# Kernel optimization log

Hardware: AMD Instinct MI355X
Metric: run time of the kernel (lower is better)

The kernel has to match this reference:

```python
import math
import jax, jax.numpy as jnp
import numpy as np

# ---- matryoshka config (matches init_kwargs) ----
NUM_HEADS = 16
KV_GROUPS = 4
KV_REPEATS = NUM_HEADS // KV_GROUPS
QK_SIZES = [32, 64, 128]      # output_sizes // num_heads
HEAD_SIZES = [32, 64, 128]
D_MODEL = 2048
NEG_INF = -1e9


def _heads_reorder_indices(num_heads, sizes, reverse=False):
    parts = [[] for _ in range(num_heads)]
    offset, prev = 0, 0
    for size in sizes:
        seg = size - prev
        for h in range(num_heads):
            parts[h].append(np.arange(offset, offset + seg))
            offset += seg
        prev = size
    reorder = np.concatenate([a for head in parts for a in head])
    if reverse:
        rev = np.empty_like(reorder)
        rev[reorder] = np.arange(len(reorder))
        reorder = rev
    return jnp.asarray(reorder, dtype=jnp.int32)

Q_REORDER = _heads_reorder_indices(NUM_HEADS, QK_SIZES)
K_REORDER = _heads_reorder_indices(KV_GROUPS, QK_SIZES)
V_REORDER = _heads_reorder_indices(KV_GROUPS, HEAD_SIZES)
O_REORDER = _heads_reorder_indices(NUM_HEADS, HEAD_SIZES, reverse=True)


def setup_inputs() -> dict:
    key = jax.random.key(0)
    ks = jax.random.split(key, 9)
    B, S = 2, 1024
    dq = NUM_HEADS * QK_SIZES[-1]      # 2048
    dkv_q = KV_GROUPS * QK_SIZES[-1]   # 512
    dkv_v = KV_GROUPS * HEAD_SIZES[-1] # 512
    dout = NUM_HEADS * HEAD_SIZES[-1]  # 2048
    s = 0.02
    return {
        "x": jax.random.normal(ks[0], (B, S, D_MODEL), jnp.float32),
        "mask": jnp.tril(jnp.ones((S, S), jnp.bool_)),
        "Wq": jax.random.normal(ks[1], (D_MODEL, dq), jnp.float32) * s,
        "bq": jnp.zeros((dq,), jnp.float32),
        "Wk": jax.random.normal(ks[2], (D_MODEL, dkv_q), jnp.float32) * s,
        "bk": jnp.zeros((dkv_q,), jnp.float32),
        "Wv": jax.random.normal(ks[3], (D_MODEL, dkv_v), jnp.float32) * s,
        "bv": jnp.zeros((dkv_v,), jnp.float32),
        "Wo": jax.random.normal(ks[4], (dout, D_MODEL), jnp.float32) * s,
        "bo": jnp.zeros((D_MODEL,), jnp.float32),
    }


def reference(x, mask, Wq, bq, Wk, bk, Wv, bv, Wo, bo):
    B, S, _ = x.shape
    H, G, R = NUM_HEADS, KV_GROUPS, KV_REPEATS
    Dq, Dh = QK_SIZES[-1], HEAD_SIZES[-1]

    # matryoshka projections (full-size forward) + buffer-indexed reorder
    q = (x @ Wq + bq)[..., Q_REORDER]
    k = (x @ Wk + bk)[..., K_REORDER]
    v = (x @ Wv + bv)[..., V_REORDER]

    q = q.reshape(B, S, H, Dq).transpose(0, 2, 1, 3)   # [B,H,S,Dq]
    k = k.reshape(B, S, G, Dq).transpose(0, 2, 1, 3)   # [B,G,S,Dq]
    v = v.reshape(B, S, G, Dh).transpose(0, 2, 1, 3)   # [B,G,S,Dh]

    # GQA expansion: each group repeated kv_repeats times consecutively
    k = jnp.repeat(k, R, axis=1)  # [B,H,S,Dq]
    v = jnp.repeat(v, R, axis=1)  # [B,H,S,Dh]

    add_mask = jnp.where(mask, 0.0, NEG_INF).astype(x.dtype)  # [S,S]

    xs = []
    dp_cum = 0.0
    prev_qk, prev_hd = 0, 0
    for qk, hd in zip(QK_SIZES, HEAD_SIZES):
        # dot product over the NEW qk segment, accumulated over prefixes
        dp = jnp.einsum('bhqd,bhkd->bhqk', q[..., prev_qk:qk], k[..., prev_qk:qk])
        dp_cum = dp_cum + dp
        logits = dp_cum * (1.0 / math.sqrt(qk)) + add_mask
        attn = jax.nn.softmax(logits, axis=-1)
        # output only the NEW value segment for this nesting level
        xs.append(jnp.einsum('bhqk,bhkd->bhqd', attn, v[..., prev_hd:hd]))
        prev_qk, prev_hd = qk, hd

    out = jnp.concatenate(xs, axis=-1)                 # [B,H,S,Dh]
    out = out.transpose(0, 2, 1, 3).reshape(B, S, H * Dh)
    out = out[..., O_REORDER]
    return out @ Wo + bo
```

## Files before the change

### kernel.cpp

```cpp
#include <hip/hip_runtime.h>

typedef __attribute__((ext_vector_type(8))) __bf16 bf16x8;
typedef __attribute__((ext_vector_type(8))) unsigned short u16x8;
typedef __attribute__((ext_vector_type(4))) float f32x4;

#define XBOFF 0
#define WQKVOFF (XBOFF + 2048 * 2048)
#define WOOFF   (WQKVOFF + 3072 * 2048)
#define QOFF    (WOOFF + 2048 * 2048)
#define KOFF    (QOFF + 2048 * 2048)
#define VTOFF   (KOFF + 2048 * 512)
#define AOFF    (VTOFF + 2048 * 512)
__device__ __align__(16) ushort g_scratch[AOFF + 2048 * 2048];

__device__ __forceinline__ int nest_map(int n, int H) {
    int h = n >> 7, j = n & 127;
    if (j < 32) return h * 32 + j;
    if (j < 64) return H * 32 + h * 32 + (j - 32);
    return H * 64 + h * 64 + (j - 64);
}

__device__ __forceinline__ ushort f2bf(float f) {
    unsigned u = __builtin_bit_cast(unsigned, f);
    u += 0x7fffu + ((u >> 16) & 1u);
    return (ushort)(u >> 16);
}
__device__ __forceinline__ bf16x8 ld_frag(const ushort* p) {
    return __builtin_bit_cast(bf16x8, *(const u16x8*)p);
}
__device__ __forceinline__ void glds16(const ushort* g, ushort* s) {
    __builtin_amdgcn_global_load_lds(
        (const __attribute__((address_space(1))) void*)g,
        (__attribute__((address_space(3))) void*)s, 16, 0, 0);
}

__global__ __launch_bounds__(256) void prep_kernel(
    const float* __restrict__ x,
    const float* __restrict__ Wq, const float* __restrict__ Wk,
    const float* __restrict__ Wv, const float* __restrict__ Wo)
{
    const int bx = blockIdx.x;
    const int tid = threadIdx.x;

    if (bx < 2048) {
        size_t i = ((size_t)bx * 256 + tid) * 8;
        float4 f0 = *(const float4*)&x[i];
        float4 f1 = *(const float4*)&x[i + 4];
        union { uint4 v; ushort u[8]; } a;
        a.u[0] = f2bf(f0.x); a.u[1] = f2bf(f0.y); a.u[2] = f2bf(f0.z); a.u[3] = f2bf(f0.w);
        a.u[4] = f2bf(f1.x); a.u[5] = f2bf(f1.y); a.u[6] = f2bf(f1.z); a.u[7] = f2bf(f1.w);
        *(uint4*)&g_scratch[XBOFF + i] = a.v;
        return;
    }

    const float* W; int rowlen, H, mode, dstoff, t;
    if (bx < 3072)      { W = Wq; rowlen = 2048; H = 16; mode = 0; dstoff = WQKVOFF;               t = bx - 2048; }
    else if (bx < 3328) { W = Wk; rowlen = 512;  H = 4;  mode = 0; dstoff = WQKVOFF + 2048 * 2048; t = bx - 3072; }
    else if (bx < 3584) { W = Wv; rowlen = 512;  H = 4;  mode = 0; dstoff = WQKVOFF + 2560 * 2048; t = bx - 3328; }
    else                { W = Wo; rowlen = 2048; H = 16; mode = 1; dstoff = WOOFF;                 t = bx - 3584; }
    const int k0 = (t & 31) * 64;
    const int n0 = (t >> 5) * 64;

    __shared__ ushort T[64][66];
    const int r = tid >> 3, oct = tid & 7;

    #pragma unroll
    for (int rep = 0; rep < 2; ++rep) {
        int rr = r + rep * 32;
        int wrow = mode ? nest_map(k0 + rr, 16) : (k0 + rr);
        int wcol = mode ? (n0 + oct * 8) : nest_map(n0 + oct * 8, H);
        float4 f0 = *(const float4*)&W[(size_t)wrow * rowlen + wcol];
        float4 f1 = *(const float4*)&W[(size_t)wrow * rowlen + wcol + 4];
        ushort* d = &T[rr][oct * 8];
        d[0] = f2bf(f0.x); d[1] = f2bf(f0.y); d[2] = f2bf(f0.z); d[3] = f2bf(f0.w);
        d[4] = f2bf(f1.x); d[5] = f2bf(f1.y); d[6] = f2bf(f1.z); d[7] = f2bf(f1.w);
    }
    __syncthreads();
    #pragma unroll
    for (int rep = 0; rep < 2; ++rep) {
        int rr = r + rep * 32;
        union { uint4 v; ushort u[8]; } cv;
        #pragma unroll
        for (int i = 0; i < 8; ++i) cv.u[i] = T[oct * 8 + i][rr];
        *(uint4*)&g_scratch[dstoff + (size_t)(n0 + rr) * 2048 + k0 + oct * 8] = cv.v;
    }
}

__global__ __launch_bounds__(256) void gemm128_kernel(
    const float* __restrict__ b0, const float* __restrict__ b1,
    const float* __restrict__ b2, float* __restrict__ oext, int mode)
{
    __shared__ __align__(16) ushort SH[2 * 12288];

    const int gx = gridDim.x;
    const int gy = gridDim.y;
    const int id = blockIdx.x + gx * blockIdx.y;
    const int xcd = id & 7, idl = id >> 3;
    const int CM = gy >> 1, CN = gx >> 2;
    const int m_idx = (xcd >> 2) * CM + (idl % CM);
    const int n_idx = (xcd & 3) * CN + (idl / CM);
    const int n0 = n_idx * 64;
    const int m0 = m_idx * 128;

    const int tid = threadIdx.x;
    const int lane = tid & 63, wid = tid >> 6;
    const int wm = wid & 1, wn = wid >> 1;
    const int quad = lane >> 4, l16 = lane & 15;

    const ushort* A  = g_scratch + (mode ? AOFF : XBOFF);
    const ushort* Bt = g_scratch + (mode ? WOOFF : WQKVOFF);

    const bool vpath = (mode == 0) && (n0 >= 2560);
    const float* bias; ushort* outS = nullptr; int c0, oldim, H;
    if (mode == 1)      { bias = b0; c0 = n0; oldim = 2048; H = 0; }
    else if (n0 < 2048) { bias = b0; outS = g_scratch + QOFF; c0 = n0;        oldim = 2048; H = 16; }
    else if (n0 < 2560) { bias = b1; outS = g_scratch + KOFF; c0 = n0 - 2048; oldim = 512;  H = 4; }
    else                { bias = b2; outS = nullptr;          c0 = n0 - 2560; oldim = 512;  H = 4; }

    const int lrow = lane >> 3;
    const int lchunk = (lane & 7) ^ (lrow & 7);

    f32x4 acc[4][2];
    #pragma unroll
    for (int a = 0; a < 4; ++a)
        #pragma unroll
        for (int c = 0; c < 2; ++c) acc[a][c] = f32x4{0.f, 0.f, 0.f, 0.f};

    auto STAGE = [&](int buf, int kt) {
        const int k0 = kt * 64;
        ushort* as_ = SH + buf * 12288;
        ushort* bs_ = as_ + 8192;
        #pragma unroll
        for (int it = 0; it < 4; ++it) {
            int rb = it * 32 + wid * 8;
            int r  = rb + lrow;
            glds16(&A[(size_t)(m0 + r) * 2048 + k0 + lchunk * 8], &as_[rb * 64]);
        }
        #pragma unroll
        for (int it = 0; it < 2; ++it) {
            int rb = it * 32 + wid * 8;
            int r  = rb + lrow;
            glds16(&Bt[(size_t)(n0 + r) * 2048 + k0 + lchunk * 8], &bs_[rb * 64]);
        }
    };

    STAGE(0, 0);
    STAGE(1, 1);

    for (int kt = 0; kt < 32; ++kt) {
        if (kt < 31) asm volatile("s_waitcnt vmcnt(6)" ::: "memory");
        else         asm volatile("s_waitcnt vmcnt(0)" ::: "memory");
        __builtin_amdgcn_s_barrier();

        const ushort* as_ = SH + (kt & 1) * 12288;
        const ushort* bs_ = as_ + 8192;
        #pragma unroll
        for (int kc = 0; kc < 2; ++kc) {
            bf16x8 af[4], bf[2];
            #pragma unroll
            for (int s = 0; s < 4; ++s) {
                int ra = wm * 64 + s * 16 + l16;
                int ch = kc * 4 + quad;
                af[s] = ld_frag(&as_[ra * 64 + ((ch ^ (ra & 7)) * 8)]);
            }
            #pragma unroll
            for (int s = 0; s < 2; ++s) {
                int rbv = wn * 32 + s * 16 + l16;
                int ch = kc * 4 + quad;
                bf[s] = ld_frag(&bs_[rbv * 64 + ((ch ^ (rbv & 7)) * 8)]);
            }
            #pragma unroll
            for (int sm = 0; sm < 4; ++sm)
                #pragma unroll
                for (int sn = 0; sn < 2; ++sn)
                    acc[sm][sn] = __builtin_amdgcn_mfma_f32_16x16x32_bf16(
                        af[sm], bf[sn], acc[sm][sn], 0, 0, 0);
        }
        __builtin_amdgcn_s_barrier();
        if (kt <= 29) STAGE(kt & 1, kt + 2);
    }
    __syncthreads();

    if (vpath) {
        #pragma unroll
        for (int sm = 0; sm < 4; ++sm)
        #pragma unroll
        for (int sn = 0; sn < 2; ++sn)
        #pragma unroll
        for (int i = 0; i < 4; ++i) {
            int r = wm * 64 + sm * 16 + quad * 4 + i;
            int loc = wn * 32 + sn * 16 + l16;
            float v = acc[sm][sn][i] + bias[nest_map(c0 + loc, 4)];
            SH[loc * 128 + (r ^ ((loc & 7) << 3))] = f2bf(v);
        }
        __syncthreads();
        const int dloc = tid >> 2;
        const int qcol = (tid & 3) * 32;
        const int gg = c0 >> 7, din = (c0 & 127);
        const int bb = m0 >> 10, sb = m0 & 1023;
        ushort* vt = g_scratch + VTOFF;
        #pragma unroll
        for (int j = 0; j < 4; ++j) {
            int r = qcol + j * 8;
            uint4 v = *(uint4*)&SH[dloc * 128 + (r ^ ((dloc & 7) << 3))];
            *(uint4*)&vt[((size_t)((bb * 4 + gg) * 128 + din + dloc)) * 1024 + sb + r] = v;
        }
    } else {
        #pragma unroll
        for (int sm = 0; sm < 4; ++sm)
        #pragma unroll
        for (int sn = 0; sn < 2; ++sn)
        #pragma unroll
        for (int i = 0; i < 4; ++i) {
            int row = m0 + wm * 64 + sm * 16 + quad * 4 + i;
            int loc = wn * 32 + sn * 16 + l16;
            float v = acc[sm][sn][i];
            if (mode == 1) {
                oext[(size_t)row * 2048 + c0 + loc] = v + bias[c0 + loc];
            } else {
                v += bias[nest_map(c0 + loc, H)];
                outS[(size_t)row * oldim + c0 + loc] = f2bf(v);
            }
        }
    }
}

__global__ __launch_bounds__(256) void attn_kernel()
{
    const ushort* qb = g_scratch + QOFF;
    const ushort* kb = g_scratch + KOFF;
    const ushort* vt = g_scratch + VTOFF;
    ushort* att = g_scratch + AOFF;

    __shared__ __align__(16) ushort Ks[64 * 128];
    __shared__ __align__(16) ushort Vt[128 * 64];
    __shared__ __align__(16) ushort Ps[64 * 64];

    const int x = blockIdx.x, h = blockIdx.y, b = blockIdx.z;
    const int ks_half = x >> 1;
    const int qt = ((x ^ b) & 1) ? ks_half : 15 - ks_half;
    const int g = h >> 2;
    const int q0 = qt * 64;
    const int tid = threadIdx.x;
    const int lane = tid & 63, w = tid >> 6;
    const int quad = lane >> 4, l16 = lane & 15;

    bf16x8 qa[4];
    {
        const ushort* qrow =
            qb + ((size_t)((b * 1024 + q0 + w * 16 + l16) * 16 + h)) * 128;
        #pragma unroll
        for (int kc = 0; kc < 4; ++kc)
            qa[kc] = ld_frag(qrow + kc * 32 + quad * 8);
    }

    float m_s[3][4], l_s[3][4];
    #pragma unroll
    for (int l = 0; l < 3; ++l)
        #pragma unroll
        for (int i = 0; i < 4; ++i) { m_s[l][i] = -1e9f; l_s[l][i] = 0.0f; }
    f32x4 oacc[8];
    #pragma unroll
    for (int t2 = 0; t2 < 8; ++t2) oacc[t2] = f32x4{0.f, 0.f, 0.f, 0.f};
    const f32x4 fz = {0.f, 0.f, 0.f, 0.f};
    const bf16x8 ones = __builtin_bit_cast(bf16x8, u16x8{
        0x3F80, 0x3F80, 0x3F80, 0x3F80, 0x3F80, 0x3F80, 0x3F80, 0x3F80});

    for (int kt = 0; kt <= qt; ++kt) {
        const int k0 = kt * 64;
        {
            int r16 = tid >> 4, oct16 = tid & 15;
            #pragma unroll
            for (int rep = 0; rep < 4; ++rep) {
                int row = r16 + rep * 16;
                *(uint4*)&Ks[row * 128 + ((oct16 ^ (row & 7)) * 8)] =
                    *(const uint4*)&kb[(size_t)((b * 1024 + k0 + row) * 4 + g) * 128 + oct16 * 8];
            }
            int oct = tid & 7, dr = tid >> 3;
            #pragma unroll
            for (int rep = 0; rep < 4; ++rep) {
                int d = dr + rep * 32;
                *(uint4*)&Vt[d * 64 + ((oct ^ (d & 7)) * 8)] =
                    *(const uint4*)&vt[((size_t)((b * 4 + g) * 128 + d)) * 1024 + k0 + oct * 8];
            }
        }
        __syncthreads();

        const bool diag = (kt == qt);

        f32x4 s0[4], s1[4], s2[4];
        __builtin_amdgcn_s_setprio(1);
        #pragma unroll
        for (int n = 0; n < 4; ++n) {
            int r = n * 16 + l16;
            s0[n] = __builtin_amdgcn_mfma_f32_16x16x32_bf16(
                qa[0], ld_frag(&Ks[r * 128 + (((0 + quad) ^ (r & 7)) * 8)]), fz, 0, 0, 0);
        }
        #pragma unroll
        for (int n = 0; n < 4; ++n) {
            int r = n * 16 + l16;
            s1[n] = __builtin_amdgcn_mfma_f32_16x16x32_bf16(
                qa[1], ld_frag(&Ks[r * 128 + (((4 + quad) ^ (r & 7)) * 8)]), s0[n], 0, 0, 0);
        }
        #pragma unroll
        for (int n = 0; n < 4; ++n) {
            int r = n * 16 + l16;
            s2[n] = __builtin_amdgcn_mfma_f32_16x16x32_bf16(
                qa[2], ld_frag(&Ks[r * 128 + (((8 + quad) ^ (r & 7)) * 8)]), s1[n], 0, 0, 0);
        }
        #pragma unroll
        for (int n = 0; n < 4; ++n) {
            int r = n * 16 + l16;
            s2[n] = __builtin_amdgcn_mfma_f32_16x16x32_bf16(
                qa[3], ld_frag(&Ks[r * 128 + (((12 + quad) ^ (r & 7)) * 8)]), s2[n], 0, 0, 0);
        }
        __builtin_amdgcn_s_setprio(0);

        float sv[3][4][4], mx[3][4];
        #pragma unroll
        for (int l = 0; l < 3; ++l)
            #pragma unroll
            for (int i = 0; i < 4; ++i) mx[l][i] = -1e9f;
        #pragma unroll
        for (int n = 0; n < 4; ++n)
            #pragma unroll
            for (int i = 0; i < 4; ++i) {
                bool msk = diag &&
                    (k0 + n * 16 + l16 > q0 + w * 16 + quad * 4 + i);
                float x0 = msk ? -1e9f : s0[n][i] * 0.1767766953f;
                float x1 = msk ? -1e9f : s1[n][i] * 0.125f;
                float x2 = msk ? -1e9f : s2[n][i] * 0.0883883476f;
                sv[0][n][i] = x0; mx[0][i] = fmaxf(mx[0][i], x0);
                sv[1][n][i] = x1; mx[1][i] = fmaxf(mx[1][i], x1);
                sv[2][n][i] = x2; mx[2][i] = fmaxf(mx[2][i], x2);
            }
        #pragma unroll
        for (int d = 1; d < 16; d <<= 1)
            #pragma unroll
            for (int l = 0; l < 3; ++l)
                #pragma unroll
                for (int i = 0; i < 4; ++i)
                    mx[l][i] = fmaxf(mx[l][i], __shfl_xor(mx[l][i], d, 64));
        float al[3][4];
        #pragma unroll
        for (int l = 0; l < 3; ++l)
            #pragma unroll
            for (int i = 0; i < 4; ++i) {
                float mn = fmaxf(m_s[l][i], mx[l][i]);
                al[l][i] = __expf(m_s[l][i] - mn);
                m_s[l][i] = mn;
            }
        #pragma unroll
        for (int n = 0; n < 4; ++n)
            #pragma unroll
            for (int l = 0; l < 3; ++l)
                #pragma unroll
                for (int i = 0; i < 4; ++i)
                    sv[l][n][i] = __expf(sv[l][n][i] - m_s[l][i]);
        #pragma unroll
        for (int t = 0; t < 8; ++t) {
            int lvl = (t < 2) ? 0 : (t < 4) ? 1 : 2;
            #pragma unroll
            for (int i = 0; i < 4; ++i) oacc[t][i] *= al[lvl][i];
        }

        f32x4 racc[3];
        const int obase[3] = {0, 2, 4}, onts[3] = {2, 2, 4}, voffs[3] = {0, 32, 64};
        #pragma unroll
        for (int l = 0; l < 3; ++l) {
            #pragma unroll
            for (int n = 0; n < 4; ++n)
                #pragma unroll
                for (int i = 0; i < 4; ++i) {
                    int prow = w * 16 + quad * 4 + i;
                    int col = n * 16 + l16;
                    Ps[prow * 64 + ((((col >> 3) ^ (prow & 7)) << 3) | (col & 7))] =
                        f2bf(sv[l][n][i]);
                }
            racc[l] = fz;
            __builtin_amdgcn_s_setprio(1);
            #pragma unroll
            for (int kc = 0; kc < 2; ++kc) {
                int prow = w * 16 + l16;
                bf16x8 pa = ld_frag(&Ps[prow * 64 + (((kc * 4 + quad) ^ (prow & 7)) * 8)]);
                racc[l] = __builtin_amdgcn_mfma_f32_16x16x32_bf16(
                    pa, ones, racc[l], 0, 0, 0);
                #pragma unroll
                for (int t = 0; t < 4; ++t) {
                    if (t < onts[l]) {
                        int vd = voffs[l] + t * 16 + l16;
                        bf16x8 vf = ld_frag(&Vt[vd * 64 + (((kc * 4 + quad) ^ (vd & 7)) * 8)]);
                        oacc[obase[l] + t] = __builtin_amdgcn_mfma_f32_16x16x32_bf16(
                            pa, vf, oacc[obase[l] + t], 0, 0, 0);
                    }
                }
            }
            __builtin_amdgcn_s_setprio(0);
        }
        #pragma unroll
        for (int l = 0; l < 3; ++l)
            #pragma unroll
            for (int i = 0; i < 4; ++i)
                l_s[l][i] = l_s[l][i] * al[l][i] + racc[l][i];
        __syncthreads();
    }

    float inv[3][4];
    #pragma unroll
    for (int l = 0; l < 3; ++l)
        #pragma unroll
        for (int i = 0; i < 4; ++i) {
            float L = l_s[l][i];
            inv[l][i] = (L > 0.f) ? (1.0f / L) : 0.f;
        }
    #pragma unroll
    for (int t = 0; t < 8; ++t) {
        int lvl = (t < 2) ? 0 : (t < 4) ? 1 : 2;
        #pragma unroll
        for (int i = 0; i < 4; ++i) {
            int srow = q0 + w * 16 + quad * 4 + i;
            att[(size_t)((b * 1024 + srow) * 16 + h) * 128 + t * 16 + l16] =
                f2bf(oacc[t][i] * inv[lvl][i]);
        }
    }
}

extern "C" void kernel_launch(void* const* d_in, const int* in_sizes, int n_in,
                              void* d_out, int out_size, void* d_ws, size_t ws_size,
                              hipStream_t stream)
{
    const float* x  = (const float*)d_in[0];
    const float* Wq = (const float*)d_in[2];
    const float* bq = (const float*)d_in[3];
    const float* Wk = (const float*)d_in[4];
    const float* bk = (const float*)d_in[5];
    const float* Wv = (const float*)d_in[6];
    const float* bv = (const float*)d_in[7];
    const float* Wo = (const float*)d_in[8];
    const float* bo = (const float*)d_in[9];
    float* out = (float*)d_out;
    (void)d_ws; (void)ws_size;

    dim3 blk(256, 1, 1);
    hipLaunchKernelGGL(prep_kernel, dim3(4608), blk, 0, stream, x, Wq, Wk, Wv, Wo);
    hipLaunchKernelGGL(gemm128_kernel, dim3(48, 16), blk, 0, stream,
                       bq, bk, bv, (float*)nullptr, 0);
    hipLaunchKernelGGL(attn_kernel, dim3(16, 16, 2), blk, 0, stream);
    hipLaunchKernelGGL(gemm128_kernel, dim3(32, 16), blk, 0, stream,
                       bo, nullptr, nullptr, out, 1);
}
```

Baseline: 261.3 us.

## Double-buffer K/V tiles in attention with async global-to-LDS loads

The attention kernel now keeps two LDS buffers each for K and V^T. The next key tile is prefetched with direct global-to-LDS loads (glds16) while the current tile is computed, and vmcnt waits plus raw s_barrier replace the register-staged copy and __syncthreads. The aim is to hide global load latency behind the MFMA work. In exchange LDS use roughly doubles, which may cut occupancy. The manual vmcnt counting is also fragile: if other outstanding loads change the count, the ordering can break.

```diff
diff --git a/kernel.cpp b/kernel.cpp
--- a/kernel.cpp
+++ b/kernel.cpp
@@ -232,8 +232,8 @@
     const ushort* vt = g_scratch + VTOFF;
     ushort* att = g_scratch + AOFF;
 
-    __shared__ __align__(16) ushort Ks[64 * 128];
-    __shared__ __align__(16) ushort Vt[128 * 64];
+    __shared__ __align__(16) ushort Ks[2][64 * 128];
+    __shared__ __align__(16) ushort Vt[2][128 * 64];
     __shared__ __align__(16) ushort Ps[64 * 64];
 
     const int x = blockIdx.x, h = blockIdx.y, b = blockIdx.z;
@@ -244,6 +244,27 @@
     const int tid = threadIdx.x;
     const int lane = tid & 63, w = tid >> 6;
     const int quad = lane >> 4, l16 = lane & 15;
+    const int w4 = w * 4, w8 = w * 8;
+
+    auto STAGE = [&](int bf, int kt) {
+        const int k0 = kt * 64;
+        #pragma unroll
+        for (int rep = 0; rep < 4; ++rep) {
+            int rowb = rep * 16 + w4;
+            int row  = rowb + (lane >> 4);
+            int c    = lane & 15;
+            glds16(&kb[(size_t)((b * 1024 + k0 + row) * 4 + g) * 128 + ((c ^ (row & 7)) * 8)],
+                   &Ks[bf][rowb * 128]);
+        }
+        #pragma unroll
+        for (int rep = 0; rep < 4; ++rep) {
+            int db = rep * 32 + w8;
+            int d  = db + (lane >> 3);
+            int c  = lane & 7;
+            glds16(&vt[((size_t)((b * 4 + g) * 128 + d)) * 1024 + k0 + ((c ^ (d & 7)) * 8)],
+                   &Vt[bf][db * 64]);
+        }
+    };
 
     bf16x8 qa[4];
     {
@@ -266,26 +287,20 @@
     const bf16x8 ones = __builtin_bit_cast(bf16x8, u16x8{
         0x3F80, 0x3F80, 0x3F80, 0x3F80, 0x3F80, 0x3F80, 0x3F80, 0x3F80});
 
+    STAGE(0, 0);
+
     for (int kt = 0; kt <= qt; ++kt) {
         const int k0 = kt * 64;
-        {
-            int r16 = tid >> 4, oct16 = tid & 15;
-            #pragma unroll
-            for (int rep = 0; rep < 4; ++rep) {
-                int row = r16 + rep * 16;
-                *(uint4*)&Ks[row * 128 + ((oct16 ^ (row & 7)) * 8)] =
-                    *(const uint4*)&kb[(size_t)((b * 1024 + k0 + row) * 4 + g) * 128 + oct16 * 8];
-            }
-            int oct = tid & 7, dr = tid >> 3;
-            #pragma unroll
-            for (int rep = 0; rep < 4; ++rep) {
-                int d = dr + rep * 32;
-                *(uint4*)&Vt[d * 64 + ((oct ^ (d & 7)) * 8)] =
-                    *(const uint4*)&vt[((size_t)((b * 4 + g) * 128 + d)) * 1024 + k0 + oct * 8];
-            }
-        }
-        __syncthreads();
-
+        if (kt < qt) {
+            STAGE((kt + 1) & 1, kt + 1);
+            asm volatile("s_waitcnt vmcnt(8)" ::: "memory");
+        } else {
+            asm volatile("s_waitcnt vmcnt(0)" ::: "memory");
+        }
+        __builtin_amdgcn_s_barrier();
+
+        const ushort* KsC = Ks[kt & 1];
+        const ushort* VtC = Vt[kt & 1];
         const bool diag = (kt == qt);
 
         f32x4 s0[4], s1[4], s2[4];
@@ -294,25 +309,25 @@
         for (int n = 0; n < 4; ++n) {
             int r = n * 16 + l16;
             s0[n] = __builtin_amdgcn_mfma_f32_16x16x32_bf16(
-                qa[0], ld_frag(&Ks[r * 128 + (((0 + quad) ^ (r & 7)) * 8)]), fz, 0, 0, 0);
+                qa[0], ld_frag(&KsC[r * 128 + (((0 + quad) ^ (r & 7)) * 8)]), fz, 0, 0, 0);
         }
         #pragma unroll
         for (int n = 0; n < 4; ++n) {
             int r = n * 16 + l16;
             s1[n] = __builtin_amdgcn_mfma_f32_16x16x32_bf16(
-                qa[1], ld_frag(&Ks[r * 128 + (((4 + quad) ^ (r & 7)) * 8)]), s0[n], 0, 0, 0);
+                qa[1], ld_frag(&KsC[r * 128 + (((4 + quad) ^ (r & 7)) * 8)]), s0[n], 0, 0, 0);
         }
         #pragma unroll
         for (int n = 0; n < 4; ++n) {
             int r = n * 16 + l16;
             s2[n] = __builtin_amdgcn_mfma_f32_16x16x32_bf16(
-                qa[2], ld_frag(&Ks[r * 128 + (((8 + quad) ^ (r & 7)) * 8)]), s1[n], 0, 0, 0);
+                qa[2], ld_frag(&KsC[r * 128 + (((8 + quad) ^ (r & 7)) * 8)]), s1[n], 0, 0, 0);
         }
         #pragma unroll
         for (int n = 0; n < 4; ++n) {
             int r = n * 16 + l16;
             s2[n] = __builtin_amdgcn_mfma_f32_16x16x32_bf16(
-                qa[3], ld_frag(&Ks[r * 128 + (((12 + quad) ^ (r & 7)) * 8)]), s2[n], 0, 0, 0);
+                qa[3], ld_frag(&KsC[r * 128 + (((12 + quad) ^ (r & 7)) * 8)]), s2[n], 0, 0, 0);
         }
         __builtin_amdgcn_s_setprio(0);
 
@@ -389,7 +404,7 @@
                 for (int t = 0; t < 4; ++t) {
                     if (t < onts[l]) {
                         int vd = voffs[l] + t * 16 + l16;
-                        bf16x8 vf = ld_frag(&Vt[vd * 64 + (((kc * 4 + quad) ^ (vd & 7)) * 8)]);
+                        bf16x8 vf = ld_frag(&VtC[vd * 64 + (((kc * 4 + quad) ^ (vd & 7)) * 8)]);
                         oacc[obase[l] + t] = __builtin_amdgcn_mfma_f32_16x16x32_bf16(
                             pa, vf, oacc[obase[l] + t], 0, 0, 0);
                     }
@@ -402,7 +417,7 @@
             #pragma unroll
             for (int i = 0; i < 4; ++i)
                 l_s[l][i] = l_s[l][i] * al[l][i] + racc[l][i];
-        __syncthreads();
+        __builtin_amdgcn_s_barrier();
     }
 
     float inv[3][4];
```

Result: slower. 282.7 us (+8.2%).
